# Optimization experiments

Measured on AMD Instinct MI355X. Metric: run time of the kernel, lower is better.

Reference implementation:

```python
import jax, jax.numpy as jnp
import numpy as np

B, C, T = 4, 80, 800            # batch, n_mels (= d_model), frames
DEPTH, D_IN, N, DT_R, K = 12, 160, 16, 5, 4  # layers, expand*d_model, d_state, dt_rank, conv kernel
ATT, EMB, EPS = 128, 192, 1e-12

LP_NAMES = ['ln1_g','ln1_b','in_proj','conv_w','conv_b','x_proj','dt_w','dt_b','A_log','D','out_proj','ln2_g','ln2_b','ff_w1','ff_b1','ff_w2','ff_b2']
PP_NAMES = ['att_w1','att_b1','bn1_g','bn1_b','bn1_m','bn1_v','att_w2','att_b2','bn2_g','bn2_b','bn2_m','bn2_v','fc_w','fc_b']


def _layernorm(x, g, b, eps=1e-5):
    mu = x.mean(-1, keepdims=True)
    v = ((x - mu) ** 2).mean(-1, keepdims=True)
    return (x - mu) * jax.lax.rsqrt(v + eps) * g + b


def _mamba(x, p):
    # x: [B, L, d_model] -> standard Mamba selective-scan block
    xz = x @ p['in_proj']                              # [B,L,2*D_IN]
    xc, z = jnp.split(xz, 2, axis=-1)
    xp = jnp.pad(xc, ((0, 0), (K - 1, 0), (0, 0)))     # causal left pad
    xc = jax.lax.conv_general_dilated(
        xp, p['conv_w'], (1,), 'VALID',
        dimension_numbers=('NWC', 'WIO', 'NWC'),
        feature_group_count=D_IN) + p['conv_b']
    xc = jax.nn.silu(xc)
    dbc = xc @ p['x_proj']                             # [B,L,DT_R+2N]
    dt, Bm, Cm = jnp.split(dbc, [DT_R, DT_R + N], axis=-1)
    dt = jax.nn.softplus(dt @ p['dt_w'] + p['dt_b'])   # [B,L,D_IN]
    A = -jnp.exp(p['A_log'])                           # [D_IN,N]

    def step(h, inp):
        x_t, dt_t, B_t, C_t = inp                      # [B,D],[B,D],[B,N],[B,N]
        dA = jnp.exp(dt_t[..., None] * A)              # [B,D,N]
        h = dA * h + (dt_t * x_t)[..., None] * B_t[:, None, :]
        y = jnp.einsum('bdn,bn->bd', h, C_t)
        return h, y

    h0 = jnp.zeros((x.shape[0], D_IN, N), x.dtype)
    xs = tuple(jnp.swapaxes(a, 0, 1) for a in (xc, dt, Bm, Cm))
    _, ys = jax.lax.scan(step, h0, xs)
    y = jnp.swapaxes(ys, 0, 1) + xc * p['D']
    y = y * jax.nn.silu(z)
    return y @ p['out_proj']


def _encoder(x, p):
    xn = _layernorm(x, p['ln1_g'], p['ln1_b'])
    fwd = _mamba(xn, p)
    bwd = jnp.flip(_mamba(jnp.flip(xn, 1), p), 1)      # bidirectional, shared weights
    m = _layernorm(fwd + bwd, p['ln2_g'], p['ln2_b'])
    ff = jax.nn.gelu(m @ p['ff_w1'] + p['ff_b1'], approximate=False) @ p['ff_w2'] + p['ff_b2']
    return ff + x


def _forward(feat, lp, pp):
    feat = feat - feat.mean(-1, keepdims=True)         # CMN
    x = jnp.swapaxes(feat, 1, 2)                       # [B,T,C]

    def body(xc, p):
        return _encoder(xc, p), None

    x, _ = jax.lax.scan(body, x, lp)                   # 12 stacked layers
    x = jnp.swapaxes(x, 1, 2)                          # [B,C,T]

    # Attentive statistics pooling (global context)
    mean = x.mean(-1, keepdims=True)
    std = jnp.sqrt(jnp.maximum(((x - mean) ** 2).mean(-1, keepdims=True), EPS))
    g = jnp.concatenate([x, jnp.broadcast_to(mean, x.shape), jnp.broadcast_to(std, x.shape)], axis=1)  # [B,3C,T]
    a = jnp.einsum('bct,cd->bdt', g, pp['att_w1']) + pp['att_b1'][:, None]
    a = jax.nn.relu(a)
    a = (a - pp['bn1_m'][:, None]) * jax.lax.rsqrt(pp['bn1_v'][:, None] + 1e-5) * pp['bn1_g'][:, None] + pp['bn1_b'][:, None]
    a = jnp.tanh(a)
    a = jnp.einsum('bdt,dc->bct', a, pp['att_w2']) + pp['att_b2'][:, None]
    w = jax.nn.softmax(a, axis=-1)
    mu = jnp.sum(w * x, axis=-1)
    sg = jnp.sqrt(jnp.maximum(jnp.sum(w * x * x, axis=-1) - mu ** 2, EPS))
    pooled = jnp.concatenate([mu, sg], axis=-1)        # [B,2C]

    pooled = (pooled - pp['bn2_m']) * jax.lax.rsqrt(pp['bn2_v'] + 1e-5) * pp['bn2_g'] + pp['bn2_b']
    return pooled @ pp['fc_w'] + pp['fc_b']            # [B,EMB] source embedding


def setup_inputs() -> dict:
    key = jax.random.key(0)
    ks = jax.random.split(key, 12)

    def w(k, shape, s=0.05):
        return jax.random.normal(k, shape, jnp.float32) * s

    L = DEPTH
    return {
        'feat': jax.random.normal(ks[0], (B, C, T), jnp.float32),
        'ln1_g': jnp.ones((L, C)), 'ln1_b': jnp.zeros((L, C)),
        'in_proj': w(ks[1], (L, C, 2 * D_IN)),
        'conv_w': w(ks[2], (L, K, 1, D_IN), 0.2),
        'conv_b': jnp.zeros((L, D_IN)),
        'x_proj': w(ks[3], (L, D_IN, DT_R + 2 * N)),
        'dt_w': w(ks[4], (L, DT_R, D_IN), 0.2),
        'dt_b': jnp.full((L, D_IN), -2.0),
        'A_log': jnp.tile(jnp.log(jnp.arange(1, N + 1, dtype=jnp.float32)), (L, D_IN, 1)),
        'D': jnp.ones((L, D_IN)),
        'out_proj': w(ks[5], (L, D_IN, C)),
        'ln2_g': jnp.ones((L, C)), 'ln2_b': jnp.zeros((L, C)),
        'ff_w1': w(ks[6], (L, C, 4 * C)), 'ff_b1': jnp.zeros((L, 4 * C)),
        'ff_w2': w(ks[7], (L, 4 * C, C)), 'ff_b2': jnp.zeros((L, C)),
        'att_w1': w(ks[8], (3 * C, ATT)), 'att_b1': jnp.zeros((ATT,)),
        'bn1_g': jnp.ones((ATT,)), 'bn1_b': jnp.zeros((ATT,)),
        'bn1_m': jnp.zeros((ATT,)), 'bn1_v': jnp.ones((ATT,)),
        'att_w2': w(ks[9], (ATT, C)), 'att_b2': jnp.zeros((C,)),
        'bn2_g': jnp.ones((2 * C,)), 'bn2_b': jnp.zeros((2 * C,)),
        'bn2_m': jnp.zeros((2 * C,)), 'bn2_v': jnp.ones((2 * C,)),
        'fc_w': w(ks[10], (2 * C, EMB)), 'fc_b': jnp.zeros((EMB,)),
        'aug': 0,
    }


def reference(feat, ln1_g, ln1_b, in_proj, conv_w, conv_b, x_proj, dt_w, dt_b, A_log, D, out_proj, ln2_g, ln2_b, ff_w1, ff_b1, ff_w2, ff_b2, att_w1, att_b1, bn1_g, bn1_b, bn1_m, bn1_v, att_w2, att_b2, bn2_g, bn2_b, bn2_m, bn2_v, fc_w, fc_b, aug):
    lp = dict(zip(LP_NAMES, (ln1_g, ln1_b, in_proj, conv_w, conv_b, x_proj, dt_w, dt_b, A_log, D, out_proj, ln2_g, ln2_b, ff_w1, ff_b1, ff_w2, ff_b2)))
    pp = dict(zip(PP_NAMES, (att_w1, att_b1, bn1_g, bn1_b, bn1_m, bn1_v, att_w2, att_b2, bn2_g, bn2_b, bn2_m, bn2_v, fc_w, fc_b)))
    # aug == 0 -> SpecAug skipped (eval path); speaker branch (frozen, no_grad) omitted
    return _forward(feat, lp, pp)
```

## Files before the change

### kernel.cpp

```cpp
#include <hip/hip_runtime.h>
#include <hip/hip_bf16.h>

#define B_ 4
#define C_ 80
#define T_ 800
#define R_ 3200
#define DIN 160
#define NST 16
#define NC 16
#define LCH 50

typedef const float* fp;

__device__ __forceinline__ void g2l16(const float* g, float* l) {
  __builtin_amdgcn_global_load_lds(
      (const __attribute__((address_space(1))) void*)g,
      (__attribute__((address_space(3))) void*)l,
      16, 0, 0);
}

__device__ __forceinline__ float blockSum(float v, float* sb) {
  for (int o = 32; o; o >>= 1) v += __shfl_xor(v, o);
  __syncthreads();
  if ((threadIdx.x & 63) == 0) sb[threadIdx.x >> 6] = v;
  __syncthreads();
  return sb[0] + sb[1] + sb[2] + sb[3];
}
__device__ __forceinline__ float blockMax(float v, float* sb) {
  for (int o = 32; o; o >>= 1) v = fmaxf(v, __shfl_xor(v, o));
  __syncthreads();
  if ((threadIdx.x & 63) == 0) sb[threadIdx.x >> 6] = v;
  __syncthreads();
  return fmaxf(fmaxf(sb[0], sb[1]), fmaxf(sb[2], sb[3]));
}

__global__ __launch_bounds__(256) void prepw_k(fp in_proj, fp ff_w1,
    fp ln1_g, fp ln1_b, fp ln2_g, fp ln2_b, fp ff_b1,
    float* __restrict__ wp, float* __restrict__ uvb) {
  int idx = blockIdx.x * 256 + threadIdx.x;
  int c = idx % 320, lm = idx / 320;
  int mat = lm & 1, l = lm >> 1;
  fp W = (mat ? ff_w1 : in_proj) + l * 25600;
  fp g = (mat ? ln2_g : ln1_g) + l * 80;
  fp b = (mat ? ln2_b : ln1_b) + l * 80;
  float* wpo = wp + lm * 25600;
  float u = 0.f, v = 0.f;
  for (int k = 0; k < 80; ++k) {
    float w = W[k * 320 + c];
    float gw = g[k] * w;
    wpo[k * 320 + c] = gw;
    u += gw;
    v += b[k] * w;
  }
  if (mat) v += ff_b1[l * 320 + c];
  uvb[lm * 640 + c] = u;
  uvb[lm * 640 + 320 + c] = v;
}

__global__ __launch_bounds__(256) void prepx_k(fp x_proj, float* __restrict__ xpt) {
  int idx = blockIdx.x * 256 + threadIdx.x;
  if (idx >= 71040) return;
  int l = idx / 5920, r = idx % 5920;
  int c = r / 160, k = r % 160;
  xpt[idx] = x_proj[l * 5920 + k * 37 + c];
}

__global__ __launch_bounds__(256) void prept_k(fp out_proj, fp ff_w2,
    float* __restrict__ wot, float* __restrict__ w2t) {
  int idx = blockIdx.x * 256 + threadIdx.x;
  if (idx < 153600) {
    int l = idx / 12800, r = idx % 12800;
    int c = r / 160, k = r % 160;
    wot[idx] = out_proj[l * 12800 + k * 80 + c];
  } else if (idx < 153600 + 307200) {
    int j = idx - 153600;
    int l = j / 25600, r = j % 25600;
    int c = r / 320, k = r % 320;
    w2t[j] = ff_w2[l * 25600 + k * 80 + c];
  }
}

__global__ __launch_bounds__(256) void cmn_k(fp feat, float* __restrict__ x) {
  int bc = blockIdx.x;
  int b = bc / C_, c = bc % C_;
  const float* f = feat + (b * C_ + c) * T_;
  __shared__ float sb[4];
  int tid = threadIdx.x;
  float v[4]; float s = 0.f;
  #pragma unroll
  for (int i = 0; i < 4; ++i) {
    int t = tid + i * 256;
    v[i] = (t < T_) ? f[t] : 0.f;
    s += v[i];
  }
  s = blockSum(s, sb);
  float mu = s * (1.f / T_);
  #pragma unroll
  for (int i = 0; i < 4; ++i) {
    int t = tid + i * 256;
    if (t < T_) x[(b * T_ + t) * C_ + c] = v[i] - mu;
  }
}

__global__ __launch_bounds__(256) void rstat_k(const float* __restrict__ in,
                                               float* __restrict__ must) {
  int row = blockIdx.x * 16 + (threadIdx.x >> 4);
  int c16 = threadIdx.x & 15;
  float s = 0.f, q = 0.f;
  #pragma unroll
  for (int m = 0; m < 5; ++m) {
    float v = in[row * 80 + c16 + 16 * m];
    s += v; q += v * v;
  }
  s += __shfl_xor(s, 1); s += __shfl_xor(s, 2);
  s += __shfl_xor(s, 4); s += __shfl_xor(s, 8);
  q += __shfl_xor(q, 1); q += __shfl_xor(q, 2);
  q += __shfl_xor(q, 4); q += __shfl_xor(q, 8);
  if (c16 == 0) {
    float mu = s * 0.0125f;
    float rs = rsqrtf(fmaxf(q * 0.0125f - mu * mu, 0.f) + 1e-5f);
    must[row * 2] = mu;
    must[row * 2 + 1] = rs;
  }
}

template<int EPI>
__global__ __launch_bounds__(256, 4) void gw_k(const float* __restrict__ A,
    fp W, fp uv, const float* __restrict__ must, const float* __restrict__ extra,
    float* __restrict__ out, int N) {
  __shared__ float SL[5120 + 4 * 1280];
  int tid = threadIdx.x, wv = tid >> 6, ln = tid & 63;
  int bid = blockIdx.x;
  int c0 = (bid / 50) * 64;
  int row0 = ((bid % 50) * 4 + wv) * 16;
  for (int ch = wv; ch < 20; ch += 4) {
    int m = ch * 256 + ln * 4;
    int kr = m >> 6, cc = m & 63;
    int lo = __builtin_amdgcn_readfirstlane(ch * 256);
    g2l16(W + kr * N + c0 + cc, SL + lo);
  }
  int abase = __builtin_amdgcn_readfirstlane(5120 + wv * 1280);
  float* As = SL + 5120 + wv * 1280;
  #pragma unroll
  for (int i = 0; i < 5; ++i) {
    int m = i * 256 + ln * 4;
    int r = m / 80, kk = m - r * 80;
    g2l16(A + (row0 + r) * 80 + kk, SL + abase + i * 256);
  }
  __syncthreads();
  int rq = ln >> 4, c16 = ln & 15;
  float acc[4][4] = {};
  #pragma unroll 2
  for (int k4 = 0; k4 < 80; k4 += 4) {
    float4 a[4], w[4];
    #pragma unroll
    for (int i = 0; i < 4; ++i)
      a[i] = *(const float4*)&As[(rq * 4 + i) * 80 + k4];
    #pragma unroll
    for (int kk = 0; kk < 4; ++kk)
      w[kk] = *(const float4*)&SL[(k4 + kk) * 64 + c16 * 4];
    #pragma unroll
    for (int i = 0; i < 4; ++i) {
      acc[i][0] += a[i].x*w[0].x + a[i].y*w[1].x + a[i].z*w[2].x + a[i].w*w[3].x;
      acc[i][1] += a[i].x*w[0].y + a[i].y*w[1].y + a[i].z*w[2].y + a[i].w*w[3].y;
      acc[i][2] += a[i].x*w[0].z + a[i].y*w[1].z + a[i].z*w[2].z + a[i].w*w[3].z;
      acc[i][3] += a[i].x*w[0].w + a[i].y*w[1].w + a[i].z*w[2].w + a[i].w*w[3].w;
    }
  }
  float ua[4], va[4];
  if (EPI != 3) {
    *(float4*)ua = *(const float4*)&uv[c0 + c16 * 4];
    *(float4*)va = *(const float4*)&uv[N + c0 + c16 * 4];
  }
  #pragma unroll
  for (int i = 0; i < 4; ++i) {
    int row = row0 + rq * 4 + i;
    float mu = 0.f, rs = 1.f;
    if (EPI != 3) {
      float2 ms = *(const float2*)&must[row * 2];
      mu = ms.x; rs = ms.y;
    }
    float4 o;
    float* op = &o.x;
    #pragma unroll
    for (int j = 0; j < 4; ++j) {
      float v = acc[i][j];
      if (EPI == 3) {
        int c = c0 + c16 * 4 + j;
        v += extra[(row / T_) * 128 + c];
        v = fmaxf(v, 0.f);
        v = v * extra[512 + c] + extra[640 + c];
        v = tanhf(v);
      } else {
        v = rs * v - mu * rs * ua[j] + va[j];
      }
      op[j] = v;
    }
    *(float4*)&out[row * N + c0 + c16 * 4] = o;
  }
}

template<int EPI, int KCH, int NKC, int SUM2, int STAT>
__global__ __launch_bounds__(256, 4) void gc_k(const float* __restrict__ A,
    fp W, fp bias, const float* __restrict__ extra, float* __restrict__ out,
    int Astride, float* __restrict__ must) {
  constexpr int P = KCH + 4;
  __shared__ float As[16 * P];
  __shared__ float Wt[80 * P];
  int tid = threadIdx.x;
  int row0 = blockIdx.x * 16;
  int rr = tid >> 4, c16 = tid & 15;
  float acc[5] = {};
  for (int kc = 0; kc < NKC; ++kc) {
    if (kc) __syncthreads();
    #pragma unroll
    for (int i = 0; i < 16 * KCH / 256; ++i) {
      int e = tid + i * 256;
      int r = e / KCH, k = e - r * KCH;
      float v;
      if (SUM2) v = A[(row0 + r) * 320 + k] + A[(row0 + r) * 320 + 160 + k];
      else      v = A[(row0 + r) * Astride + kc * KCH + k];
      As[r * P + k] = v;
    }
    #pragma unroll
    for (int i = 0; i < KCH * 80 / 256; ++i) {
      int e = tid + i * 256;
      int kr = e / 80, c = e - kr * 80;
      Wt[c * P + kr] = W[(kc * KCH + kr) * 80 + c];
    }
    __syncthreads();
    #pragma unroll 4
    for (int k4 = 0; k4 < KCH; k4 += 4) {
      float4 a = *(const float4*)&As[rr * P + k4];
      #pragma unroll
      for (int m = 0; m < 5; ++m) {
        float4 w = *(const float4*)&Wt[(c16 + 16 * m) * P + k4];
        acc[m] += a.x * w.x + a.y * w.y + a.z * w.z + a.w * w.w;
      }
    }
  }
  int row = row0 + rr;
  #pragma unroll
  for (int m = 0; m < 5; ++m) {
    int c = c16 + 16 * m;
    float v = acc[m];
    if (EPI == 2) v += bias[c] + extra[row * 80 + c];
    else if (EPI == 4) v += bias[c];
    out[row * 80 + c] = v;
  }
}

__global__ __launch_bounds__(256, 2) void gof_k(const float* __restrict__ yg,
    fp wotl, fp w1pl, fp uv1, float* __restrict__ g1) {
  __shared__ float As[16 * 164];
  __shared__ float Wt[80 * 164];
  __shared__ float sl[16 * 84];
  __shared__ float ss[32];
  int tid = threadIdx.x, row0 = blockIdx.x * 16, rr = tid >> 4, c16 = tid & 15;
  #pragma unroll
  for (int i = 0; i < 10; ++i) {
    int e = tid + i * 256; int r = e / 160, k = e - r * 160;
    As[r * 164 + k] = yg[(row0 + r) * 320 + k] + yg[(row0 + r) * 320 + 160 + k];
  }
  #pragma unroll
  for (int i = 0; i < 50; ++i) {
    int e = tid + i * 256; int c = e / 160, k = e - c * 160;
    Wt[c * 164 + k] = wotl[e];
  }
  __syncthreads();
  float acc[5] = {};
  #pragma unroll 4
  for (int k4 = 0; k4 < 160; k4 += 4) {
    float4 a = *(const float4*)&As[rr * 164 + k4];
    #pragma unroll
    for (int m = 0; m < 5; ++m) {
      float4 w = *(const float4*)&Wt[(c16 + 16 * m) * 164 + k4];
      acc[m] += a.x * w.x + a.y * w.y + a.z * w.z + a.w * w.w;
    }
  }
  float s = 0.f, q = 0.f;
  #pragma unroll
  for (int m = 0; m < 5; ++m) {
    float v = acc[m];
    sl[rr * 84 + c16 + 16 * m] = v;
    s += v; q += v * v;
  }
  s += __shfl_xor(s, 1); s += __shfl_xor(s, 2);
  s += __shfl_xor(s, 4); s += __shfl_xor(s, 8);
  q += __shfl_xor(q, 1); q += __shfl_xor(q, 2);
  q += __shfl_xor(q, 4); q += __shfl_xor(q, 8);
  if (c16 == 0) {
    float mu = s * 0.0125f;
    ss[rr * 2] = mu;
    ss[rr * 2 + 1] = rsqrtf(fmaxf(q * 0.0125f - mu * mu, 0.f) + 1e-5f);
  }
  for (int h = 0; h < 2; ++h) {
    __syncthreads();
    #pragma unroll
    for (int i = 0; i < 50; ++i) {
      int e = tid + i * 256; int kr = e / 160, c = e - kr * 160;
      Wt[kr * 164 + c] = w1pl[kr * 320 + h * 160 + c];
    }
    __syncthreads();
    float mu = ss[rr * 2], rs = ss[rr * 2 + 1];
    float a2[10] = {};
    for (int k = 0; k < 80; k += 4) {
      float4 av = *(const float4*)&sl[rr * 84 + k];
      #pragma unroll
      for (int m = 0; m < 10; ++m) {
        int c = c16 + 16 * m;
        a2[m] += av.x * Wt[k * 164 + c] + av.y * Wt[(k + 1) * 164 + c]
               + av.z * Wt[(k + 2) * 164 + c] + av.w * Wt[(k + 3) * 164 + c];
      }
    }
    #pragma unroll
    for (int m = 0; m < 10; ++m) {
      int c = h * 160 + c16 + 16 * m;
      float v = rs * a2[m] - mu * rs * uv1[c] + uv1[320 + c];
      v = 0.5f * v * (1.f + erff(v * 0.70710678118f));
      g1[(row0 + rr) * 320 + c] = v;
    }
  }
}

template<int LAST>
__global__ __launch_bounds__(256, 2) void gfi_k(const float* __restrict__ g1,
    fp w2tl, fp fb2, float* __restrict__ x, fp wpn, fp uvn,
    float* __restrict__ xz) {
  __shared__ float As[16 * 164];
  __shared__ float Wt[80 * 164];
  __shared__ float xn[16 * 84];
  __shared__ float ss[32];
  int tid = threadIdx.x, row0 = blockIdx.x * 16, rr = tid >> 4, c16 = tid & 15;
  float acc[5] = {};
  for (int kc = 0; kc < 2; ++kc) {
    if (kc) __syncthreads();
    #pragma unroll
    for (int i = 0; i < 10; ++i) {
      int e = tid + i * 256; int r = e / 160, k = e - r * 160;
      As[r * 164 + k] = g1[(row0 + r) * 320 + kc * 160 + k];
    }
    #pragma unroll
    for (int i = 0; i < 50; ++i) {
      int e = tid + i * 256; int c = e / 160, k = e - c * 160;
      Wt[c * 164 + k] = w2tl[c * 320 + kc * 160 + k];
    }
    __syncthreads();
    #pragma unroll 4
    for (int k4 = 0; k4 < 160; k4 += 4) {
      float4 a = *(const float4*)&As[rr * 164 + k4];
      #pragma unroll
      for (int m = 0; m < 5; ++m) {
        float4 w = *(const float4*)&Wt[(c16 + 16 * m) * 164 + k4];
        acc[m] += a.x * w.x + a.y * w.y + a.z * w.z + a.w * w.w;
      }
    }
  }
  float s = 0.f, q = 0.f;
  #pragma unroll
  for (int m = 0; m < 5; ++m) {
    int c = c16 + 16 * m;
    float v = acc[m] + fb2[c] + x[(row0 + rr) * 80 + c];
    x[(row0 + rr) * 80 + c] = v;
    xn[rr * 84 + c] = v;
    s += v; q += v * v;
  }
  if (!LAST) {
    s += __shfl_xor(s, 1); s += __shfl_xor(s, 2);
    s += __shfl_xor(s, 4); s += __shfl_xor(s, 8);
    q += __shfl_xor(q, 1); q += __shfl_xor(q, 2);
    q += __shfl_xor(q, 4); q += __shfl_xor(q, 8);
    if (c16 == 0) {
      float mu = s * 0.0125f;
      ss[rr * 2] = mu;
      ss[rr * 2 + 1] = rsqrtf(fmaxf(q * 0.0125f - mu * mu, 0.f) + 1e-5f);
    }
    for (int h = 0; h < 2; ++h) {
      __syncthreads();
      #pragma unroll
      for (int i = 0; i < 50; ++i) {
        int e = tid + i * 256; int kr = e / 160, c = e - kr * 160;
        Wt[kr * 164 + c] = wpn[kr * 320 + h * 160 + c];
      }
      __syncthreads();
      float mu = ss[rr * 2], rs = ss[rr * 2 + 1];
      float a2[10] = {};
      for (int k = 0; k < 80; k += 4) {
        float4 av = *(const float4*)&xn[rr * 84 + k];
        #pragma unroll
        for (int m = 0; m < 10; ++m) {
          int c = c16 + 16 * m;
          a2[m] += av.x * Wt[k * 164 + c] + av.y * Wt[(k + 1) * 164 + c]
                 + av.z * Wt[(k + 2) * 164 + c] + av.w * Wt[(k + 3) * 164 + c];
        }
      }
      #pragma unroll
      for (int m = 0; m < 10; ++m) {
        int c = h * 160 + c16 + 16 * m;
        xz[(row0 + rr) * 320 + c] = rs * a2[m] - mu * rs * uvn[c] + uvn[320 + c];
      }
    }
  }
}

__global__ __launch_bounds__(256) void cxf_k(const float* __restrict__ xz,
    fp cw, fp cb, fp xptl, fp dtw, fp dtb,
    float* __restrict__ xcf, float* __restrict__ xcbb,
    float* __restrict__ dbc2, float* __restrict__ dt2) {
  __shared__ float As[16 * 164];
  __shared__ float xpT[37 * 164];
  __shared__ float dbcl[16 * 40];
  int bi = blockIdx.x;
  int tc = bi % 50; int rem = bi / 50;
  int b = rem & 3, dir = rem >> 2;
  int t0 = tc * 16;
  int tid = threadIdx.x;
  #pragma unroll
  for (int i = 0; i < 24; ++i) {
    int e = tid + i * 256;
    if (e < 5920) {
      int c = e / 160, k = e - c * 160;
      xpT[c * 164 + k] = xptl[e];
    }
  }
  float* xco = dir ? xcbb : xcf;
  #pragma unroll
  for (int i = 0; i < 3; ++i) {
    int e = tid + i * 256;
    if (e < 640) {
      int ii = e / 40, d4 = (e - ii * 40) * 4;
      int t = t0 + ii;
      float4 acc = *(const float4*)&cb[d4];
      #pragma unroll
      for (int k = 0; k < 4; ++k) {
        int tt = t - 3 + k;
        if (tt >= 0) {
          int src = dir ? (T_ - 1 - tt) : tt;
          float4 xv = *(const float4*)&xz[(b * T_ + src) * 320 + d4];
          float4 wv = *(const float4*)&cw[k * DIN + d4];
          acc.x += wv.x * xv.x; acc.y += wv.y * xv.y;
          acc.z += wv.z * xv.z; acc.w += wv.w * xv.w;
        }
      }
      float4 o;
      o.x = acc.x / (1.f + __expf(-acc.x));
      o.y = acc.y / (1.f + __expf(-acc.y));
      o.z = acc.z / (1.f + __expf(-acc.z));
      o.w = acc.w / (1.f + __expf(-acc.w));
      *(float4*)&As[ii * 164 + d4] = o;
      *(float4*)&xco[(b * T_ + t) * DIN + d4] = o;
    }
  }
  __syncthreads();
  int rr = tid >> 4, c16 = tid & 15;
  int grow0 = dir * R_ + b * T_ + t0;
  {
    float a0 = 0.f, a1 = 0.f, a2 = 0.f;
    for (int k4 = 0; k4 < 160; k4 += 4) {
      float4 a = *(const float4*)&As[rr * 164 + k4];
      float4 w0 = *(const float4*)&xpT[c16 * 164 + k4];
      float4 w1 = *(const float4*)&xpT[(c16 + 16) * 164 + k4];
      a0 += a.x * w0.x + a.y * w0.y + a.z * w0.z + a.w * w0.w;
      a1 += a.x * w1.x + a.y * w1.y + a.z * w1.z + a.w * w1.w;
      if (c16 < 5) {
        float4 w2 = *(const float4*)&xpT[(c16 + 32) * 164 + k4];
        a2 += a.x * w2.x + a.y * w2.y + a.z * w2.z + a.w * w2.w;
      }
    }
    dbcl[rr * 40 + c16] = a0;
    dbcl[rr * 40 + c16 + 16] = a1;
    dbc2[(grow0 + rr) * 37 + c16] = a0;
    dbc2[(grow0 + rr) * 37 + c16 + 16] = a1;
    if (c16 < 5) {
      dbcl[rr * 40 + c16 + 32] = a2;
      dbc2[(grow0 + rr) * 37 + c16 + 32] = a2;
    }
  }
  __syncthreads();
  #pragma unroll
  for (int i = 0; i < 10; ++i) {
    int e = tid + i * 256;
    int ii = e / 160, d = e - ii * 160;
    float v = dtb[d];
    #pragma unroll
    for (int m = 0; m < 5; ++m) v += dbcl[ii * 40 + m] * dtw[m * DIN + d];
    v = fmaxf(v, 0.f) + __logf(1.f + __expf(-fabsf(v)));
    dt2[(grow0 + ii) * DIN + d] = v;
  }
}

__global__ __launch_bounds__(256) void scanA_k(const float* __restrict__ dt2,
    const float* __restrict__ xcf, const float* __restrict__ xcbb,
    const float* __restrict__ dbc2, fp A_log,
    float* __restrict__ hend, float* __restrict__ pprod) {
  int bi = blockIdx.x;
  int cch = bi % NC; int rem = bi / NC;
  int dblk = rem % 10; rem /= 10;
  int b = rem % 4; int dir = rem / 4;
  int d0 = dblk * 16;
  int tid = threadIdx.x, dl = tid >> 4, n = tid & 15;
  int d = d0 + dl;
  float Areg = -__expf(A_log[d * NST + n]);
  __shared__ float sdt[LCH][16], sdx[LCH][16], sB[LCH][16];
  const float* xc = dir ? xcbb : xcf;
  int rbase = dir * R_ + b * T_ + cch * LCH;
  int rloc0 = b * T_ + cch * LCH;
  for (int e = tid; e < LCH * 16; e += 256) {
    int i = e >> 4, jj = e & 15;
    int grow = rbase + i;
    float dtv = dt2[grow * DIN + d0 + jj];
    sdt[i][jj] = dtv;
    sdx[i][jj] = dtv * xc[(rloc0 + i) * DIN + d0 + jj];
    sB[i][jj]  = dbc2[grow * 37 + 5 + jj];
  }
  __syncthreads();
  float h = 0.f, dts = 0.f;
  #pragma unroll 2
  for (int i = 0; i < LCH; ++i) {
    float dtv = sdt[i][dl];
    float a = __expf(dtv * Areg);
    h = a * h + sdx[i][dl] * sB[i][n];
    dts += dtv;
  }
  hend[bi * 256 + tid] = h;
  pprod[bi * 256 + tid] = __expf(dts * Areg);
}

__global__ __launch_bounds__(256) void scanC_k(const float* __restrict__ dt2,
    const float* __restrict__ dbc2, const float* __restrict__ xcf,
    const float* __restrict__ xcbb, const float* __restrict__ xz,
    fp A_log, fp Dp, const float* __restrict__ hend,
    const float* __restrict__ pprod, float* __restrict__ ygcat) {
  int bi = blockIdx.x;
  int cch = bi % NC; int rem = bi / NC;
  int dblk = rem % 10; rem /= 10;
  int b = rem % 4; int dir = rem / 4;
  int d0 = dblk * 16;
  int tid = threadIdx.x, dl = tid >> 4, n = tid & 15;
  int d = d0 + dl;
  float Areg = -__expf(A_log[d * NST + n]);
  __shared__ float sdt[LCH][16], sdx[LCH][16], sB[LCH][16], sC[LCH][16];
  __shared__ float sY[LCH][16];
  const float* xc = dir ? xcbb : xcf;
  int rbase = dir * R_ + b * T_ + cch * LCH;
  int rloc0 = b * T_ + cch * LCH;
  int sbase = (bi / NC) * (NC * 256) + tid;
  float h = 0.f;
  #pragma unroll
  for (int cc = 0; cc < NC; ++cc) {
    float p = pprod[sbase + cc * 256];
    float e = hend[sbase + cc * 256];
    if (cc < cch) h = p * h + e;
  }
  for (int e = tid; e < LCH * 16; e += 256) {
    int i = e >> 4, jj = e & 15;
    int grow = rbase + i;
    float dtv = dt2[grow * DIN + d0 + jj];
    sdt[i][jj] = dtv;
    sdx[i][jj] = dtv * xc[(rloc0 + i) * DIN + d0 + jj];
    sB[i][jj]  = dbc2[grow * 37 + 5 + jj];
    sC[i][jj]  = dbc2[grow * 37 + 21 + jj];
  }
  __syncthreads();
  for (int i = 0; i < LCH; ++i) {
    float a = __expf(sdt[i][dl] * Areg);
    h = a * h + sdx[i][dl] * sB[i][n];
    float y = h * sC[i][n];
    y += __shfl_xor(y, 1);
    y += __shfl_xor(y, 2);
    y += __shfl_xor(y, 4);
    y += __shfl_xor(y, 8);
    if (n == 0) sY[i][dl] = y;
  }
  __syncthreads();
  for (int e = tid; e < LCH * 16; e += 256) {
    int i = e >> 4, jj = e & 15;
    int t = cch * LCH + i;
    int rloc = b * T_ + t;
    float xcv = xc[rloc * DIN + d0 + jj];
    int orow = dir ? (b * T_ + (T_ - 1 - t)) : rloc;
    float z = xz[orow * 320 + 160 + d0 + jj];
    float sg = 1.f / (1.f + __expf(-z));
    ygcat[orow * 320 + dir * 160 + d0 + jj] = (sY[i][jj] + xcv * Dp[d0 + jj]) * (z * sg);
  }
}

__global__ __launch_bounds__(256) void stats_k(const float* __restrict__ x,
                                               float* __restrict__ meanv, float* __restrict__ stdv) {
  int bc = blockIdx.x; int b = bc / C_, c = bc % C_;
  __shared__ float sb[4];
  int tid = threadIdx.x;
  float v[4]; float s = 0.f;
  #pragma unroll
  for (int i = 0; i < 4; ++i) {
    int t = tid + i * 256;
    v[i] = (t < T_) ? x[(b * T_ + t) * C_ + c] : 0.f;
    s += v[i];
  }
  s = blockSum(s, sb);
  float mu = s * (1.f / T_);
  float q = 0.f;
  #pragma unroll
  for (int i = 0; i < 4; ++i) {
    int t = tid + i * 256;
    if (t < T_) { float dd = v[i] - mu; q += dd * dd; }
  }
  q = blockSum(q, sb);
  if (tid == 0) { meanv[bc] = mu; stdv[bc] = sqrtf(fmaxf(q * (1.f / T_), 1e-12f)); }
}

__global__ __launch_bounds__(256) void prep_k(const float* __restrict__ meanv,
    const float* __restrict__ stdv, fp w1, fp ab1, fp g1p, fp b1p, fp m1p, fp v1p,
    float* __restrict__ pack) {
  int idx = blockIdx.x * 256 + threadIdx.x;
  if (idx < 512) {
    int b = idx / 128, dcol = idx % 128;
    float acc = ab1[dcol];
    for (int c = 0; c < C_; ++c) {
      acc += meanv[b * C_ + c] * w1[(C_ + c) * 128 + dcol];
      acc += stdv[b * C_ + c] * w1[(2 * C_ + c) * 128 + dcol];
    }
    pack[idx] = acc;
  } else if (idx < 640) {
    int dcol = idx - 512;
    float kv = g1p[dcol] * rsqrtf(v1p[dcol] + 1e-5f);
    pack[512 + dcol] = kv;
    pack[640 + dcol] = b1p[dcol] - m1p[dcol] * kv;
  }
}

__global__ __launch_bounds__(256) void pool_k(const float* __restrict__ x,
    const float* __restrict__ scores, fp g2, fp b2, fp m2, fp v2,
    float* __restrict__ pooledn) {
  int bc = blockIdx.x; int b = bc / C_, c = bc % C_;
  __shared__ float sb[4];
  int tid = threadIdx.x;
  float sv[4], xv[4];
  float mx = -1e30f;
  #pragma unroll
  for (int i = 0; i < 4; ++i) {
    int t = tid + i * 256;
    if (t < T_) { sv[i] = scores[(b * T_ + t) * C_ + c]; xv[i] = x[(b * T_ + t) * C_ + c]; }
    else { sv[i] = -1e30f; xv[i] = 0.f; }
    mx = fmaxf(mx, sv[i]);
  }
  mx = blockMax(mx, sb);
  float se = 0.f, sx = 0.f, sxx = 0.f;
  #pragma unroll
  for (int i = 0; i < 4; ++i) {
    float e = expf(sv[i] - mx);
    se += e; sx += e * xv[i]; sxx += e * xv[i] * xv[i];
  }
  se = blockSum(se, sb);
  sx = blockSum(sx, sb);
  sxx = blockSum(sxx, sb);
  if (tid == 0) {
    float mu = sx / se;
    float sg = sqrtf(fmaxf(sxx / se - mu * mu, 1e-12f));
    int j0 = c, j1 = C_ + c;
    pooledn[b * 160 + j0] = (mu - m2[j0]) * rsqrtf(v2[j0] + 1e-5f) * g2[j0] + b2[j0];
    pooledn[b * 160 + j1] = (sg - m2[j1]) * rsqrtf(v2[j1] + 1e-5f) * g2[j1] + b2[j1];
  }
}

__global__ __launch_bounds__(256) void fc_k(const float* __restrict__ pooledn, fp fw, fp fb,
                                            float* __restrict__ out) {
  int idx = blockIdx.x * 256 + threadIdx.x;
  if (idx >= 4 * 192) return;
  int b = idx / 192, e = idx % 192;
  float acc = fb[e];
  for (int i = 0; i < 160; ++i) acc += pooledn[b * 160 + i] * fw[i * 192 + e];
  out[idx] = acc;
}

extern "C" void kernel_launch(void* const* d_in, const int* in_sizes, int n_in,
                              void* d_out, int out_size, void* d_ws, size_t ws_size,
                              hipStream_t stream) {
  fp feat   = (fp)d_in[0];
  fp ln1_g  = (fp)d_in[1];  fp ln1_b  = (fp)d_in[2];
  fp in_proj= (fp)d_in[3];
  fp conv_w = (fp)d_in[4];  fp conv_b = (fp)d_in[5];
  fp x_proj = (fp)d_in[6];
  fp dt_w   = (fp)d_in[7];  fp dt_b   = (fp)d_in[8];
  fp A_log  = (fp)d_in[9];  fp Dp     = (fp)d_in[10];
  fp out_proj=(fp)d_in[11];
  fp ln2_g  = (fp)d_in[12]; fp ln2_b  = (fp)d_in[13];
  fp ff_w1  = (fp)d_in[14]; fp ff_b1  = (fp)d_in[15];
  fp ff_w2  = (fp)d_in[16]; fp ff_b2  = (fp)d_in[17];
  fp att_w1 = (fp)d_in[18]; fp att_b1 = (fp)d_in[19];
  fp bn1_g  = (fp)d_in[20]; fp bn1_b  = (fp)d_in[21];
  fp bn1_m  = (fp)d_in[22]; fp bn1_v  = (fp)d_in[23];
  fp att_w2 = (fp)d_in[24]; fp att_b2 = (fp)d_in[25];
  fp bn2_g  = (fp)d_in[26]; fp bn2_b  = (fp)d_in[27];
  fp bn2_m  = (fp)d_in[28]; fp bn2_v  = (fp)d_in[29];
  fp fc_w   = (fp)d_in[30]; fp fc_b   = (fp)d_in[31];

  float* ws   = (float*)d_ws;
  float* x    = ws;
  float* xz   = ws + 256000;
  float* xcf  = ws + 1280000;
  float* xcb  = ws + 1792000;
  float* dbc2 = ws + 2304000;
  float* dt2  = ws + 2540800;
  float* hend = ws + 3564800;
  float* pprod= ws + 3892480;
  float* ygcat= ws + 4220160;
  float* meanv= ws + 5244160;
  float* stdv = ws + 5244480;
  float* pack = ws + 5244800;
  float* pooledn = ws + 5245568;
  float* wp   = ws + 5246208;
  float* uvb  = ws + 5860608;
  float* mst_x= ws + 5875968;
  float* xpt  = ws + 5882368;
  float* wot  = ws + 5953408;
  float* w2t  = ws + 6107008;
  float* g1   = xz;
  float* a1b  = hend;
  float* sc   = dt2;

  prepw_k<<<30, 256, 0, stream>>>(in_proj, ff_w1, ln1_g, ln1_b, ln2_g, ln2_b,
                                  ff_b1, wp, uvb);
  prepx_k<<<278, 256, 0, stream>>>(x_proj, xpt);
  prept_k<<<1800, 256, 0, stream>>>(out_proj, ff_w2, wot, w2t);
  cmn_k<<<320, 256, 0, stream>>>(feat, x);
  rstat_k<<<200, 256, 0, stream>>>(x, mst_x);
  gw_k<0><<<250, 256, 0, stream>>>(x, wp, uvb, mst_x, nullptr, xz, 320);

  for (int l = 0; l < 12; ++l) {
    cxf_k<<<400, 256, 0, stream>>>(xz, conv_w + l * 640, conv_b + l * 160,
                                   xpt + l * 5920, dt_w + l * 800, dt_b + l * 160,
                                   xcf, xcb, dbc2, dt2);
    scanA_k<<<1280, 256, 0, stream>>>(dt2, xcf, xcb, dbc2, A_log + l * 2560, hend, pprod);
    scanC_k<<<1280, 256, 0, stream>>>(dt2, dbc2, xcf, xcb, xz, A_log + l * 2560,
                                      Dp + l * 160, hend, pprod, ygcat);
    gof_k<<<200, 256, 0, stream>>>(ygcat, wot + l * 12800, wp + (2 * l + 1) * 25600,
                                   uvb + (2 * l + 1) * 640, g1);
    if (l < 11)
      gfi_k<0><<<200, 256, 0, stream>>>(g1, w2t + l * 25600, ff_b2 + l * 80, x,
                                        wp + (2 * l + 2) * 25600,
                                        uvb + (2 * l + 2) * 640, xz);
    else
      gfi_k<1><<<200, 256, 0, stream>>>(g1, w2t + l * 25600, ff_b2 + l * 80, x,
                                        wp, uvb, xz);
  }

  stats_k<<<320, 256, 0, stream>>>(x, meanv, stdv);
  prep_k<<<3, 256, 0, stream>>>(meanv, stdv, att_w1, att_b1, bn1_g, bn1_b, bn1_m, bn1_v, pack);
  gw_k<3><<<100, 256, 0, stream>>>(x, att_w1, nullptr, nullptr, pack, a1b, 128);
  gc_k<4, 128, 1, 0, 0><<<200, 256, 0, stream>>>(a1b, att_w2, att_b2, nullptr, sc, 128, nullptr);
  pool_k<<<320, 256, 0, stream>>>(x, sc, bn2_g, bn2_b, bn2_m, bn2_v, pooledn);
  fc_k<<<3, 256, 0, stream>>>(pooledn, fc_w, fc_b, (float*)d_out);
}
```

Before: 1.262 ms.

## Fuse chunk-scan pass into conv kernel, add carry kernel, merge out/FFN GEMMs

The first selective-scan pass now runs inside the conv/x_proj kernel on 16-frame chunks that are already in LDS, so scanA and its global reloads go away. A small scanB kernel propagates chunk carries serially across 50 chunks. scanC is replaced by a finer 4000-block kernel that reads precomputed start states. The out_proj+FFN1 and FFN2+next-LN kernels are merged into one kernel that keeps the GELU activations in LDS, removing a global round trip and one launch per layer. The cost is higher LDS use (about 89KB per block), more workspace for hstart, and a serial 50-step carry pass.

```diff
diff --git a/kernel.cpp b/kernel.cpp
--- a/kernel.cpp
+++ b/kernel.cpp
@@ -7,8 +7,8 @@
 #define R_ 3200
 #define DIN 160
 #define NST 16
-#define NC 16
-#define LCH 50
+#define NCH 50
+#define LCH 16
 
 typedef const float* fp;
 
@@ -200,10 +200,9 @@
   }
 }
 
-template<int EPI, int KCH, int NKC, int SUM2, int STAT>
+template<int EPI, int KCH, int NKC>
 __global__ __launch_bounds__(256, 4) void gc_k(const float* __restrict__ A,
-    fp W, fp bias, const float* __restrict__ extra, float* __restrict__ out,
-    int Astride, float* __restrict__ must) {
+    fp W, fp bias, float* __restrict__ out, int Astride) {
   constexpr int P = KCH + 4;
   __shared__ float As[16 * P];
   __shared__ float Wt[80 * P];
@@ -217,10 +216,7 @@
     for (int i = 0; i < 16 * KCH / 256; ++i) {
       int e = tid + i * 256;
       int r = e / KCH, k = e - r * KCH;
-      float v;
-      if (SUM2) v = A[(row0 + r) * 320 + k] + A[(row0 + r) * 320 + 160 + k];
-      else      v = A[(row0 + r) * Astride + kc * KCH + k];
-      As[r * P + k] = v;
+      As[r * P + k] = A[(row0 + r) * Astride + kc * KCH + k];
     }
     #pragma unroll
     for (int i = 0; i < KCH * 80 / 256; ++i) {
@@ -244,23 +240,26 @@
   for (int m = 0; m < 5; ++m) {
     int c = c16 + 16 * m;
     float v = acc[m];
-    if (EPI == 2) v += bias[c] + extra[row * 80 + c];
-    else if (EPI == 4) v += bias[c];
+    if (EPI == 4) v += bias[c];
     out[row * 80 + c] = v;
   }
 }
 
-__global__ __launch_bounds__(256, 2) void gof_k(const float* __restrict__ yg,
-    fp wotl, fp w1pl, fp uv1, float* __restrict__ g1) {
-  __shared__ float As[16 * 164];
-  __shared__ float Wt[80 * 164];
-  __shared__ float sl[16 * 84];
-  __shared__ float ss[32];
+template<int LAST>
+__global__ __launch_bounds__(256) void gfu_k(const float* __restrict__ yg,
+    fp wotl, fp w1pl, fp uv1, fp w2tl, fp fb2, float* __restrict__ x,
+    fp wpn, fp uvn, float* __restrict__ xz) {
+  __shared__ float S[22240];
+  float* Wt  = S;
+  float* AsX = S + 13120;
+  float* g1l = S + 15744;
+  float* sl  = S + 20864;
+  float* ss  = S + 22208;
   int tid = threadIdx.x, row0 = blockIdx.x * 16, rr = tid >> 4, c16 = tid & 15;
   #pragma unroll
   for (int i = 0; i < 10; ++i) {
     int e = tid + i * 256; int r = e / 160, k = e - r * 160;
-    As[r * 164 + k] = yg[(row0 + r) * 320 + k] + yg[(row0 + r) * 320 + 160 + k];
+    AsX[r * 164 + k] = yg[(row0 + r) * 320 + k] + yg[(row0 + r) * 320 + 160 + k];
   }
   #pragma unroll
   for (int i = 0; i < 50; ++i) {
@@ -268,31 +267,33 @@
     Wt[c * 164 + k] = wotl[e];
   }
   __syncthreads();
-  float acc[5] = {};
-  #pragma unroll 4
-  for (int k4 = 0; k4 < 160; k4 += 4) {
-    float4 a = *(const float4*)&As[rr * 164 + k4];
+  {
+    float acc[5] = {};
+    #pragma unroll 4
+    for (int k4 = 0; k4 < 160; k4 += 4) {
+      float4 a = *(const float4*)&AsX[rr * 164 + k4];
+      #pragma unroll
+      for (int m = 0; m < 5; ++m) {
+        float4 w = *(const float4*)&Wt[(c16 + 16 * m) * 164 + k4];
+        acc[m] += a.x * w.x + a.y * w.y + a.z * w.z + a.w * w.w;
+      }
+    }
+    float s = 0.f, q = 0.f;
     #pragma unroll
     for (int m = 0; m < 5; ++m) {
-      float4 w = *(const float4*)&Wt[(c16 + 16 * m) * 164 + k4];
-      acc[m] += a.x * w.x + a.y * w.y + a.z * w.z + a.w * w.w;
-    }
-  }
-  float s = 0.f, q = 0.f;
-  #pragma unroll
-  for (int m = 0; m < 5; ++m) {
-    float v = acc[m];
-    sl[rr * 84 + c16 + 16 * m] = v;
-    s += v; q += v * v;
-  }
-  s += __shfl_xor(s, 1); s += __shfl_xor(s, 2);
-  s += __shfl_xor(s, 4); s += __shfl_xor(s, 8);
-  q += __shfl_xor(q, 1); q += __shfl_xor(q, 2);
-  q += __shfl_xor(q, 4); q += __shfl_xor(q, 8);
-  if (c16 == 0) {
-    float mu = s * 0.0125f;
-    ss[rr * 2] = mu;
-    ss[rr * 2 + 1] = rsqrtf(fmaxf(q * 0.0125f - mu * mu, 0.f) + 1e-5f);
+      float v = acc[m];
+      sl[rr * 84 + c16 + 16 * m] = v;
+      s += v; q += v * v;
+    }
+    s += __shfl_xor(s, 1); s += __shfl_xor(s, 2);
+    s += __shfl_xor(s, 4); s += __shfl_xor(s, 8);
+    q += __shfl_xor(q, 1); q += __shfl_xor(q, 2);
+    q += __shfl_xor(q, 4); q += __shfl_xor(q, 8);
+    if (c16 == 0) {
+      float mu = s * 0.0125f;
+      ss[rr * 2] = mu;
+      ss[rr * 2 + 1] = rsqrtf(fmaxf(q * 0.0125f - mu * mu, 0.f) + 1e-5f);
+    }
   }
   for (int h = 0; h < 2; ++h) {
     __syncthreads();
@@ -318,28 +319,12 @@
       int c = h * 160 + c16 + 16 * m;
       float v = rs * a2[m] - mu * rs * uv1[c] + uv1[320 + c];
       v = 0.5f * v * (1.f + erff(v * 0.70710678118f));
-      g1[(row0 + rr) * 320 + c] = v;
-    }
-  }
-}
-
-template<int LAST>
-__global__ __launch_bounds__(256, 2) void gfi_k(const float* __restrict__ g1,
-    fp w2tl, fp fb2, float* __restrict__ x, fp wpn, fp uvn,
-    float* __restrict__ xz) {
-  __shared__ float As[16 * 164];
-  __shared__ float Wt[80 * 164];
-  __shared__ float xn[16 * 84];
-  __shared__ float ss[32];
-  int tid = threadIdx.x, row0 = blockIdx.x * 16, rr = tid >> 4, c16 = tid & 15;
-  float acc[5] = {};
+      g1l[rr * 320 + c] = v;
+    }
+  }
+  float acc2[5] = {};
   for (int kc = 0; kc < 2; ++kc) {
-    if (kc) __syncthreads();
-    #pragma unroll
-    for (int i = 0; i < 10; ++i) {
-      int e = tid + i * 256; int r = e / 160, k = e - r * 160;
-      As[r * 164 + k] = g1[(row0 + r) * 320 + kc * 160 + k];
-    }
+    __syncthreads();
     #pragma unroll
     for (int i = 0; i < 50; ++i) {
       int e = tid + i * 256; int c = e / 160, k = e - c * 160;
@@ -348,33 +333,37 @@
     __syncthreads();
     #pragma unroll 4
     for (int k4 = 0; k4 < 160; k4 += 4) {
-      float4 a = *(const float4*)&As[rr * 164 + k4];
+      float4 a = *(const float4*)&g1l[rr * 320 + kc * 160 + k4];
       #pragma unroll
       for (int m = 0; m < 5; ++m) {
         float4 w = *(const float4*)&Wt[(c16 + 16 * m) * 164 + k4];
-        acc[m] += a.x * w.x + a.y * w.y + a.z * w.z + a.w * w.w;
-      }
-    }
-  }
-  float s = 0.f, q = 0.f;
-  #pragma unroll
-  for (int m = 0; m < 5; ++m) {
-    int c = c16 + 16 * m;
-    float v = acc[m] + fb2[c] + x[(row0 + rr) * 80 + c];
-    x[(row0 + rr) * 80 + c] = v;
-    xn[rr * 84 + c] = v;
-    s += v; q += v * v;
+        acc2[m] += a.x * w.x + a.y * w.y + a.z * w.z + a.w * w.w;
+      }
+    }
+  }
+  {
+    float s = 0.f, q = 0.f;
+    #pragma unroll
+    for (int m = 0; m < 5; ++m) {
+      int c = c16 + 16 * m;
+      float v = acc2[m] + fb2[c] + x[(row0 + rr) * 80 + c];
+      x[(row0 + rr) * 80 + c] = v;
+      AsX[rr * 84 + c] = v;
+      s += v; q += v * v;
+    }
+    if (!LAST) {
+      s += __shfl_xor(s, 1); s += __shfl_xor(s, 2);
+      s += __shfl_xor(s, 4); s += __shfl_xor(s, 8);
+      q += __shfl_xor(q, 1); q += __shfl_xor(q, 2);
+      q += __shfl_xor(q, 4); q += __shfl_xor(q, 8);
+      if (c16 == 0) {
+        float mu = s * 0.0125f;
+        ss[rr * 2] = mu;
+        ss[rr * 2 + 1] = rsqrtf(fmaxf(q * 0.0125f - mu * mu, 0.f) + 1e-5f);
+      }
+    }
   }
   if (!LAST) {
-    s += __shfl_xor(s, 1); s += __shfl_xor(s, 2);
-    s += __shfl_xor(s, 4); s += __shfl_xor(s, 8);
-    q += __shfl_xor(q, 1); q += __shfl_xor(q, 2);
-    q += __shfl_xor(q, 4); q += __shfl_xor(q, 8);
-    if (c16 == 0) {
-      float mu = s * 0.0125f;
-      ss[rr * 2] = mu;
-      ss[rr * 2 + 1] = rsqrtf(fmaxf(q * 0.0125f - mu * mu, 0.f) + 1e-5f);
-    }
     for (int h = 0; h < 2; ++h) {
       __syncthreads();
       #pragma unroll
@@ -384,32 +373,34 @@
       }
       __syncthreads();
       float mu = ss[rr * 2], rs = ss[rr * 2 + 1];
-      float a2[10] = {};
+      float a3[10] = {};
       for (int k = 0; k < 80; k += 4) {
-        float4 av = *(const float4*)&xn[rr * 84 + k];
+        float4 av = *(const float4*)&AsX[rr * 84 + k];
         #pragma unroll
         for (int m = 0; m < 10; ++m) {
           int c = c16 + 16 * m;
-          a2[m] += av.x * Wt[k * 164 + c] + av.y * Wt[(k + 1) * 164 + c]
+          a3[m] += av.x * Wt[k * 164 + c] + av.y * Wt[(k + 1) * 164 + c]
                  + av.z * Wt[(k + 2) * 164 + c] + av.w * Wt[(k + 3) * 164 + c];
         }
       }
       #pragma unroll
       for (int m = 0; m < 10; ++m) {
         int c = h * 160 + c16 + 16 * m;
-        xz[(row0 + rr) * 320 + c] = rs * a2[m] - mu * rs * uvn[c] + uvn[320 + c];
-      }
-    }
-  }
-}
-
-__global__ __launch_bounds__(256) void cxf_k(const float* __restrict__ xz,
-    fp cw, fp cb, fp xptl, fp dtw, fp dtb,
+        xz[(row0 + rr) * 320 + c] = rs * a3[m] - mu * rs * uvn[c] + uvn[320 + c];
+      }
+    }
+  }
+}
+
+__global__ __launch_bounds__(256) void cxfA_k(const float* __restrict__ xz,
+    fp cw, fp cb, fp xptl, fp dtw, fp dtb, fp A_log,
     float* __restrict__ xcf, float* __restrict__ xcbb,
-    float* __restrict__ dbc2, float* __restrict__ dt2) {
+    float* __restrict__ dbc2, float* __restrict__ dt2,
+    float* __restrict__ hend, float* __restrict__ pprod) {
   __shared__ float As[16 * 164];
   __shared__ float xpT[37 * 164];
   __shared__ float dbcl[16 * 40];
+  __shared__ float dtl[16 * 164];
   int bi = blockIdx.x;
   int tc = bi % 50; int rem = bi / 50;
   int b = rem & 3, dir = rem >> 2;
@@ -485,85 +476,79 @@
     #pragma unroll
     for (int m = 0; m < 5; ++m) v += dbcl[ii * 40 + m] * dtw[m * DIN + d];
     v = fmaxf(v, 0.f) + __logf(1.f + __expf(-fabsf(v)));
+    dtl[ii * 164 + d] = v;
     dt2[(grow0 + ii) * DIN + d] = v;
   }
-}
-
-__global__ __launch_bounds__(256) void scanA_k(const float* __restrict__ dt2,
-    const float* __restrict__ xcf, const float* __restrict__ xcbb,
-    const float* __restrict__ dbc2, fp A_log,
-    float* __restrict__ hend, float* __restrict__ pprod) {
-  int bi = blockIdx.x;
-  int cch = bi % NC; int rem = bi / NC;
-  int dblk = rem % 10; rem /= 10;
-  int b = rem % 4; int dir = rem / 4;
-  int d0 = dblk * 16;
-  int tid = threadIdx.x, dl = tid >> 4, n = tid & 15;
-  int d = d0 + dl;
-  float Areg = -__expf(A_log[d * NST + n]);
-  __shared__ float sdt[LCH][16], sdx[LCH][16], sB[LCH][16];
-  const float* xc = dir ? xcbb : xcf;
-  int rbase = dir * R_ + b * T_ + cch * LCH;
-  int rloc0 = b * T_ + cch * LCH;
-  for (int e = tid; e < LCH * 16; e += 256) {
-    int i = e >> 4, jj = e & 15;
-    int grow = rbase + i;
-    float dtv = dt2[grow * DIN + d0 + jj];
-    sdt[i][jj] = dtv;
-    sdx[i][jj] = dtv * xc[(rloc0 + i) * DIN + d0 + jj];
-    sB[i][jj]  = dbc2[grow * 37 + 5 + jj];
-  }
-  __syncthreads();
-  float h = 0.f, dts = 0.f;
-  #pragma unroll 2
-  for (int i = 0; i < LCH; ++i) {
-    float dtv = sdt[i][dl];
-    float a = __expf(dtv * Areg);
-    h = a * h + sdx[i][dl] * sB[i][n];
-    dts += dtv;
-  }
-  hend[bi * 256 + tid] = h;
-  pprod[bi * 256 + tid] = __expf(dts * Areg);
-}
-
-__global__ __launch_bounds__(256) void scanC_k(const float* __restrict__ dt2,
+  __syncthreads();
+  int dl = tid >> 4, n = tid & 15;
+  (void)dl; (void)n;
+  float h[10], dts[10], Ar[10];
+  #pragma unroll
+  for (int k = 0; k < 10; ++k) {
+    Ar[k] = -__expf(A_log[k * 256 + tid]);
+    h[k] = 0.f; dts[k] = 0.f;
+  }
+  for (int i = 0; i < 16; ++i) {
+    float Bv = dbcl[i * 40 + 5 + (tid & 15)];
+    #pragma unroll
+    for (int k = 0; k < 10; ++k) {
+      int d = k * 16 + (tid >> 4);
+      float dtv = dtl[i * 164 + d];
+      float a = __expf(dtv * Ar[k]);
+      h[k] = a * h[k] + dtv * As[i * 164 + d] * Bv;
+      dts[k] += dtv;
+    }
+  }
+  int gb = (dir * 4 + b) * 10;
+  #pragma unroll
+  for (int k = 0; k < 10; ++k) {
+    int idx = ((gb + k) * NCH + tc) * 256 + tid;
+    hend[idx] = h[k];
+    pprod[idx] = __expf(dts[k] * Ar[k]);
+  }
+}
+
+__global__ __launch_bounds__(256) void scanB_k(const float* __restrict__ hend,
+    const float* __restrict__ pprod, float* __restrict__ hstart) {
+  int grp = blockIdx.x;
+  int tid = threadIdx.x;
+  int base = grp * NCH * 256 + tid;
+  float h = 0.f;
+  for (int cc = 0; cc < NCH; ++cc) {
+    hstart[base + cc * 256] = h;
+    h = pprod[base + cc * 256] * h + hend[base + cc * 256];
+  }
+}
+
+__global__ __launch_bounds__(256) void scanC16_k(const float* __restrict__ dt2,
     const float* __restrict__ dbc2, const float* __restrict__ xcf,
     const float* __restrict__ xcbb, const float* __restrict__ xz,
-    fp A_log, fp Dp, const float* __restrict__ hend,
-    const float* __restrict__ pprod, float* __restrict__ ygcat) {
+    fp A_log, fp Dp, const float* __restrict__ hstart,
+    float* __restrict__ ygcat) {
+  __shared__ float sdt[16][16], sdx[16][16], sB[16][16], sC[16][16], sY[16][16];
   int bi = blockIdx.x;
-  int cch = bi % NC; int rem = bi / NC;
-  int dblk = rem % 10; rem /= 10;
-  int b = rem % 4; int dir = rem / 4;
+  int cc = bi % NCH, grp = bi / NCH;
+  int dblk = grp % 10; int rem = grp / 10;
+  int b = rem & 3, dir = rem >> 2;
   int d0 = dblk * 16;
-  int tid = threadIdx.x, dl = tid >> 4, n = tid & 15;
-  int d = d0 + dl;
-  float Areg = -__expf(A_log[d * NST + n]);
-  __shared__ float sdt[LCH][16], sdx[LCH][16], sB[LCH][16], sC[LCH][16];
-  __shared__ float sY[LCH][16];
+  int tid = threadIdx.x, i16 = tid >> 4, jj = tid & 15;
   const float* xc = dir ? xcbb : xcf;
-  int rbase = dir * R_ + b * T_ + cch * LCH;
-  int rloc0 = b * T_ + cch * LCH;
-  int sbase = (bi / NC) * (NC * 256) + tid;
-  float h = 0.f;
-  #pragma unroll
-  for (int cc = 0; cc < NC; ++cc) {
-    float p = pprod[sbase + cc * 256];
-    float e = hend[sbase + cc * 256];
-    if (cc < cch) h = p * h + e;
-  }
-  for (int e = tid; e < LCH * 16; e += 256) {
-    int i = e >> 4, jj = e & 15;
-    int grow = rbase + i;
+  int t0 = cc * 16;
+  {
+    int grow = dir * R_ + b * T_ + t0 + i16;
+    int rloc = b * T_ + t0 + i16;
     float dtv = dt2[grow * DIN + d0 + jj];
-    sdt[i][jj] = dtv;
-    sdx[i][jj] = dtv * xc[(rloc0 + i) * DIN + d0 + jj];
-    sB[i][jj]  = dbc2[grow * 37 + 5 + jj];
-    sC[i][jj]  = dbc2[grow * 37 + 21 + jj];
-  }
-  __syncthreads();
-  for (int i = 0; i < LCH; ++i) {
-    float a = __expf(sdt[i][dl] * Areg);
+    sdt[i16][jj] = dtv;
+    sdx[i16][jj] = dtv * xc[rloc * DIN + d0 + jj];
+    sB[i16][jj] = dbc2[grow * 37 + 5 + jj];
+    sC[i16][jj] = dbc2[grow * 37 + 21 + jj];
+  }
+  float h = hstart[bi * 256 + tid];
+  float Ar = -__expf(A_log[d0 * 16 + tid]);
+  __syncthreads();
+  int dl = i16, n = jj;
+  for (int i = 0; i < 16; ++i) {
+    float a = __expf(sdt[i][dl] * Ar);
     h = a * h + sdx[i][dl] * sB[i][n];
     float y = h * sC[i][n];
     y += __shfl_xor(y, 1);
@@ -573,15 +558,14 @@
     if (n == 0) sY[i][dl] = y;
   }
   __syncthreads();
-  for (int e = tid; e < LCH * 16; e += 256) {
-    int i = e >> 4, jj = e & 15;
-    int t = cch * LCH + i;
-    int rloc = b * T_ + t;
-    float xcv = xc[rloc * DIN + d0 + jj];
-    int orow = dir ? (b * T_ + (T_ - 1 - t)) : rloc;
+  {
+    int t = t0 + i16;
+    int rl = b * T_ + t;
+    float xcv = xc[rl * DIN + d0 + jj];
+    int orow = dir ? (b * T_ + (T_ - 1 - t)) : rl;
     float z = xz[orow * 320 + 160 + d0 + jj];
     float sg = 1.f / (1.f + __expf(-z));
-    ygcat[orow * 320 + dir * 160 + d0 + jj] = (sY[i][jj] + xcv * Dp[d0 + jj]) * (z * sg);
+    ygcat[orow * 320 + dir * 160 + d0 + jj] = (sY[i16][jj] + xcv * Dp[d0 + jj]) * (z * sg);
   }
 }
 
@@ -703,19 +687,19 @@
   float* dbc2 = ws + 2304000;
   float* dt2  = ws + 2540800;
   float* hend = ws + 3564800;
-  float* pprod= ws + 3892480;
-  float* ygcat= ws + 4220160;
-  float* meanv= ws + 5244160;
-  float* stdv = ws + 5244480;
-  float* pack = ws + 5244800;
-  float* pooledn = ws + 5245568;
-  float* wp   = ws + 5246208;
-  float* uvb  = ws + 5860608;
-  float* mst_x= ws + 5875968;
-  float* xpt  = ws + 5882368;
-  float* wot  = ws + 5953408;
-  float* w2t  = ws + 6107008;
-  float* g1   = xz;
+  float* pprod= ws + 4588800;
+  float* hstart=ws + 5612800;
+  float* ygcat= ws + 6636800;
+  float* meanv= ws + 7660800;
+  float* stdv = ws + 7661120;
+  float* pack = ws + 7661440;
+  float* pooledn = ws + 7662208;
+  float* wp   = ws + 7662848;
+  float* uvb  = ws + 8277248;
+  float* mst_x= ws + 8292608;
+  float* xpt  = ws + 8299008;
+  float* wot  = ws + 8370048;
+  float* w2t  = ws + 8523648;
   float* a1b  = hend;
   float* sc   = dt2;
 
@@ -728,27 +712,33 @@
   gw_k<0><<<250, 256, 0, stream>>>(x, wp, uvb, mst_x, nullptr, xz, 320);
 
   for (int l = 0; l < 12; ++l) {
-    cxf_k<<<400, 256, 0, stream>>>(xz, conv_w + l * 640, conv_b + l * 160,
-                                   xpt + l * 5920, dt_w + l * 800, dt_b + l * 160,
-                                   xcf, xcb, dbc2, dt2);
-    scanA_k<<<1280, 256, 0, stream>>>(dt2, xcf, xcb, dbc2, A_log + l * 2560, hend, pprod);
-    scanC_k<<<1280, 256, 0, stream>>>(dt2, dbc2, xcf, xcb, xz, A_log + l * 2560,
-                                      Dp + l * 160, hend, pprod, ygcat);
-    gof_k<<<200, 256, 0, stream>>>(ygcat, wot + l * 12800, wp + (2 * l + 1) * 25600,
-                                   uvb + (2 * l + 1) * 640, g1);
+    cxfA_k<<<400, 256, 0, stream>>>(xz, conv_w + l * 640, conv_b + l * 160,
+                                    xpt + l * 5920, dt_w + l * 800, dt_b + l * 160,
+                                    A_log + l * 2560, xcf, xcb, dbc2, dt2,
+                                    hend, pprod);
+    scanB_k<<<80, 256, 0, stream>>>(hend, pprod, hstart);
+    scanC16_k<<<4000, 256, 0, stream>>>(dt2, dbc2, xcf, xcb, xz,
+                                        A_log + l * 2560, Dp + l * 160,
+                                        hstart, ygcat);
     if (l < 11)
-      gfi_k<0><<<200, 256, 0, stream>>>(g1, w2t + l * 25600, ff_b2 + l * 80, x,
+      gfu_k<0><<<200, 256, 0, stream>>>(ygcat, wot + l * 12800,
+                                        wp + (2 * l + 1) * 25600,
+                                        uvb + (2 * l + 1) * 640,
+                                        w2t + l * 25600, ff_b2 + l * 80, x,
                                         wp + (2 * l + 2) * 25600,
                                         uvb + (2 * l + 2) * 640, xz);
     else
-      gfi_k<1><<<200, 256, 0, stream>>>(g1, w2t + l * 25600, ff_b2 + l * 80, x,
+      gfu_k<1><<<200, 256, 0, stream>>>(ygcat, wot + l * 12800,
+                                        wp + (2 * l + 1) * 25600,
+                                        uvb + (2 * l + 1) * 640,
+                                        w2t + l * 25600, ff_b2 + l * 80, x,
                                         wp, uvb, xz);
   }
 
   stats_k<<<320, 256, 0, stream>>>(x, meanv, stdv);
   prep_k<<<3, 256, 0, stream>>>(meanv, stdv, att_w1, att_b1, bn1_g, bn1_b, bn1_m, bn1_v, pack);
   gw_k<3><<<100, 256, 0, stream>>>(x, att_w1, nullptr, nullptr, pack, a1b, 128);
-  gc_k<4, 128, 1, 0, 0><<<200, 256, 0, stream>>>(a1b, att_w2, att_b2, nullptr, sc, 128, nullptr);
+  gc_k<4, 128, 1><<<200, 256, 0, stream>>>(a1b, att_w2, att_b2, sc, 128);
   pool_k<<<320, 256, 0, stream>>>(x, sc, bn2_g, bn2_b, bn2_m, bn2_v, pooledn);
   fc_k<<<3, 256, 0, stream>>>(pooledn, fc_w, fc_b, (float*)d_out);
 }
```

Result: slower. 1.430 ms (+13.4%).
